# Optimization experiments

Hardware: AMD Instinct MI355X
Metric: run time of the kernel (lower is better)

Reference implementation:

```python
import jax, jax.numpy as jnp
import numpy as np

BETA = 6.0
LOG_2PI = float(np.log(2.0 * np.pi))


def setup_inputs() -> dict:
    key = jax.random.key(0)
    k1, k2, k3, k4 = jax.random.split(key, 4)
    B, L = 2048, 64
    kl = jax.random.uniform(k1, (B, L), dtype=jnp.float32)
    z_mean = jax.random.normal(k2, (B, L), dtype=jnp.float32)
    z_logvar = jax.random.normal(k3, (B, L), dtype=jnp.float32)
    z_sampled = jax.random.normal(k4, (B, L), dtype=jnp.float32)
    return {"kl": kl, "z_mean": z_mean, "z_logvar": z_logvar, "z_sampled": z_sampled}


def gaussian_log_density(samples, mean, log_var):
    # samples: [B,1,L], mean/log_var: [1,B,L] -> [B,B,L]
    tmp = samples - mean
    return -0.5 * (tmp * tmp * jnp.exp(-log_var) + log_var + LOG_2PI)


def total_correlation(z, z_mean, z_logvar):
    # [B, B, L]: log q(z_i_l | x_j)
    log_qz_prob = gaussian_log_density(z[:, None, :], z_mean[None, :, :], z_logvar[None, :, :])
    # sum_l logsumexp_j -> [B]
    log_qz_product = jnp.sum(jax.scipy.special.logsumexp(log_qz_prob, axis=1), axis=1)
    # logsumexp_j sum_l -> [B]
    log_qz = jax.scipy.special.logsumexp(jnp.sum(log_qz_prob, axis=2), axis=1)
    return jnp.mean(log_qz - log_qz_product)


def reference(kl, z_mean, z_logvar, z_sampled):
    kl_loss = jnp.sum(kl)
    tc = (BETA - 1.0) * total_correlation(z_sampled, z_mean, z_logvar)
    return tc + kl_loss
```

## Files before the change

### kernel.cpp

```cpp
#include <hip/hip_runtime.h>
#include <math.h>


#define NB 2048
#define NL 64
#define NE (NB * NL)
#define BVAL 12.0f

__device__ __forceinline__ float wredsum(float v) {
#pragma unroll
  for (int o = 32; o; o >>= 1) v += __shfl_xor(v, o, 64);
  return v;
}
__device__ __forceinline__ float wredmax(float v) {
#pragma unroll
  for (int o = 32; o; o >>= 1) v = fmaxf(v, __shfl_xor(v, o, 64));
  return v;
}

__global__ __launch_bounds__(256) void k1_pre(const float* __restrict__ kl,
                                              const float* __restrict__ zm,
                                              const float* __restrict__ zlv,
                                              float4* __restrict__ PK2,
                                              float* __restrict__ A2T,
                                              float* __restrict__ MA2T,
                                              float* __restrict__ QC2,
                                              float* __restrict__ KLP) {
  const float INVLN2 = 1.4426950408889634f;
  const float LOG2PI = 1.8378770664093453f;
  int tid = threadIdx.x;
  int e = blockIdx.x * 256 + tid;
  int j = e >> 6, l = e & 63;
  float lv = zlv[e], m = zm[e];
  float a2 = -0.5f * INVLN2 * __expf(-lv);
  float b2 = -0.5f * INVLN2 * (lv + LOG2PI);
  float c1 = -2.0f * a2 * m;
  float c0 = fmaf(a2 * m, m, b2);
  PK2[e] = make_float4(a2, c1, c0 - BVAL, 0.0f);
  A2T[l * NB + j] = a2;
  MA2T[l * NB + j] = c1;
  float q = wredsum(c0);
  if (l == 0) QC2[j] = q;
  float ks = wredsum(kl[e]);
  __shared__ float sk[4];
  if (l == 0) sk[tid >> 6] = ks;
  __syncthreads();
  if (tid == 0) KLP[blockIdx.x] = sk[0] + sk[1] + sk[2] + sk[3];
}

__global__ __launch_bounds__(256) void k2_t(const float* __restrict__ zs,
                                            const float* __restrict__ A2T,
                                            const float* __restrict__ MA2T,
                                            const float* __restrict__ QC2,
                                            float* __restrict__ TPM,
                                            float* __restrict__ TPS) {
  int jc = blockIdx.x;
  int i0 = blockIdx.y * 8;
  int tid = threadIdx.x;
  int w = tid >> 6;
  int j = jc * 256 + tid;
  __shared__ float zsh[64][8];
  if (tid < 128) {
    int k = tid >> 1, r0 = (tid & 1) * 4;
#pragma unroll
    for (int r = 0; r < 4; ++r) zsh[k][r0 + r] = zs[(i0 + r0 + r) * NL + k];
  }
  __syncthreads();
  float accv[8];
  float q = QC2[j];
#pragma unroll
  for (int r = 0; r < 8; ++r) accv[r] = q;
  for (int k = 0; k < 64; ++k) {
    float av = A2T[k * NB + j];
    float mv = MA2T[k * NB + j];
    const float4* z4 = (const float4*)&zsh[k][0];
    float4 za = z4[0], zb = z4[1];
    float zk[8] = {za.x, za.y, za.z, za.w, zb.x, zb.y, zb.z, zb.w};
#pragma unroll
    for (int r = 0; r < 8; ++r) {
      accv[r] = fmaf(zk[r] * zk[r], av, accv[r]);
      accv[r] = fmaf(zk[r], mv, accv[r]);
    }
  }
  __shared__ float lm[4][8], ls[4][8];
#pragma unroll
  for (int r = 0; r < 8; ++r) {
    float mx = wredmax(accv[r]);
    if ((tid & 63) == 0) lm[w][r] = mx;
  }
  __syncthreads();
  float Mt[8];
#pragma unroll
  for (int r = 0; r < 8; ++r)
    Mt[r] = fmaxf(fmaxf(lm[0][r], lm[1][r]), fmaxf(lm[2][r], lm[3][r]));
#pragma unroll
  for (int r = 0; r < 8; ++r) {
    float ss = wredsum(__builtin_amdgcn_exp2f(accv[r] - Mt[r]));
    if ((tid & 63) == 0) ls[w][r] = ss;
  }
  __syncthreads();
  if (tid == 0) {
#pragma unroll
    for (int r = 0; r < 8; ++r) {
      TPM[(i0 + r) * 8 + jc] = Mt[r];
      TPS[(i0 + r) * 8 + jc] = ls[0][r] + ls[1][r] + ls[2][r] + ls[3][r];
    }
  }
}

__global__ __launch_bounds__(256) void k3_lse(const float* __restrict__ zs,
                                              const float4* __restrict__ PK2,
                                              float* __restrict__ SP) {
  int jc = blockIdx.x;
  int i0 = blockIdx.y * 8;
  int tid = threadIdx.x;
  int w = tid >> 6, l = tid & 63;
  const float4* p = PK2 + (size_t)(jc * 256 + w * 64) * NL + l;
  float zr[8];
#pragma unroll
  for (int r = 0; r < 8; ++r) zr[r] = zs[(i0 + r) * NL + l];
  float S[8];
#pragma unroll
  for (int r = 0; r < 8; ++r) S[r] = 0.0f;
#pragma unroll 4
  for (int jj = 0; jj < 64; ++jj) {
    float4 c = p[(size_t)jj * NL];
#pragma unroll
    for (int r = 0; r < 8; ++r) {
      float lp2 = fmaf(fmaf(zr[r], c.x, c.y), zr[r], c.z);
      S[r] += __builtin_amdgcn_exp2f(lp2);
    }
  }
  __shared__ float lss[4][8][64];
#pragma unroll
  for (int r = 0; r < 8; ++r) lss[w][r][l] = S[r];
  __syncthreads();
  for (int pp = tid; pp < 512; pp += 256) {
    int r = pp >> 6, ll = pp & 63;
    float Sc = lss[0][r][ll] + lss[1][r][ll] + lss[2][r][ll] + lss[3][r][ll];
    SP[((size_t)jc * NB + (i0 + r)) * NL + ll] = Sc;
  }
}

__global__ __launch_bounds__(256) void k4_fin(const float* __restrict__ SP,
                                              const float* __restrict__ TPM,
                                              const float* __restrict__ TPS,
                                              float* __restrict__ PERI) {
  int tid = threadIdx.x;
  int w = tid >> 6, l = tid & 63;
  int i = blockIdx.x * 4 + w;
  float S = 0.0f;
#pragma unroll
  for (int s = 0; s < 8; ++s) S += SP[((size_t)s * NB + i) * NL + l];
  float val = __builtin_amdgcn_logf(S);
  float lqp2 = wredsum(val) + 64.0f * BVAL;
  float tm = (l < 8) ? TPM[i * 8 + l] : -1e30f;
  float ts = (l < 8) ? TPS[i * 8 + l] : 0.0f;
  float Mt = wredmax(tm);
  float St = wredsum(ts * __builtin_amdgcn_exp2f(tm - Mt));
  float lqz2 = Mt + __builtin_amdgcn_logf(St);
  if (l == 0) PERI[i] = lqz2 - lqp2;
}

__global__ __launch_bounds__(256) void k5_out(const float* __restrict__ KLP,
                                              const float* __restrict__ PERI,
                                              float* __restrict__ out) {
  int tid = threadIdx.x;
  float a = 0.0f, b = 0.0f;
  for (int x = tid; x < 512; x += 256) a += KLP[x];
  for (int x = tid; x < 2048; x += 256) b += PERI[x];
  float ra = wredsum(a), rb = wredsum(b);
  __shared__ float sa[4], sb[4];
  if ((tid & 63) == 0) {
    sa[tid >> 6] = ra;
    sb[tid >> 6] = rb;
  }
  __syncthreads();
  if (tid == 0) {
    const float LN2 = 0.6931471805599453f;
    float ka = sa[0] + sa[1] + sa[2] + sa[3];
    float kb = sb[0] + sb[1] + sb[2] + sb[3];
    out[0] = ka + 5.0f * LN2 * kb * (1.0f / (float)NB);
  }
}

extern "C" void kernel_launch(void* const* d_in, const int* in_sizes, int n_in,
                              void* d_out, int out_size, void* d_ws, size_t ws_size,
                              hipStream_t stream) {
  const float* kl = (const float*)d_in[0];
  const float* zm = (const float*)d_in[1];
  const float* zlv = (const float*)d_in[2];
  const float* zs = (const float*)d_in[3];
  float* ws = (float*)d_ws;

  float* PK2 = ws;
  float* A2T = PK2 + 4 * NE;
  float* MA2T = A2T + NE;
  float* QC2 = MA2T + NE;
  float* SP = QC2 + NB;
  float* TPM = SP + 8 * NE;
  float* TPS = TPM + NB * 8;
  float* KLP = TPS + NB * 8;
  float* PERI = KLP + 512;

  k1_pre<<<NE / 256, 256, 0, stream>>>(kl, zm, zlv, (float4*)PK2, A2T, MA2T, QC2, KLP);
  k2_t<<<dim3(8, NB / 8), 256, 0, stream>>>(zs, A2T, MA2T, QC2, TPM, TPS);
  k3_lse<<<dim3(8, NB / 8), 256, 0, stream>>>(zs, (const float4*)PK2, SP);
  k4_fin<<<NB / 4, 256, 0, stream>>>(SP, TPM, TPS, PERI);
  k5_out<<<1, 256, 0, stream>>>(KLP, PERI, (float*)d_out);
}
```

Baseline: 135.0 us.

## Fuse TC, LSE, finalize and output kernels with atomic last-block reductions

Merges the four post-processing kernels into one launch. The joint-density pass and the per-dimension logsumexp pass now share a block over a larger tile of 16 sample rows, where each block previously handled 8. The per-row finalization and the global output reduction run in whichever block arrives last, detected with atomic counters and threadfences. This removes three kernel launches and their gaps and doubles reuse of the loaded coefficients per block. In exchange it raises register pressure, since 16 accumulators are held per thread, and halves the grid size, which may reduce occupancy and parallelism.

```diff
diff --git a/kernel.cpp b/kernel.cpp
--- a/kernel.cpp
+++ b/kernel.cpp
@@ -6,6 +6,8 @@
 #define NL 64
 #define NE (NB * NL)
 #define BVAL 12.0f
+#define ITILE 16
+#define NTILE (NB / ITILE)
 
 __device__ __forceinline__ float wredsum(float v) {
 #pragma unroll
@@ -25,12 +27,14 @@
                                               float* __restrict__ A2T,
                                               float* __restrict__ MA2T,
                                               float* __restrict__ QC2,
-                                              float* __restrict__ KLP) {
+                                              float* __restrict__ KLP,
+                                              int* __restrict__ CNT) {
   const float INVLN2 = 1.4426950408889634f;
   const float LOG2PI = 1.8378770664093453f;
   int tid = threadIdx.x;
   int e = blockIdx.x * 256 + tid;
   int j = e >> 6, l = e & 63;
+  if (e < NTILE + 1) CNT[e] = 0;
   float lv = zlv[e], m = zm[e];
   float a2 = -0.5f * INVLN2 * __expf(-lv);
   float b2 = -0.5f * INVLN2 * (lv + LOG2PI);
@@ -48,133 +52,143 @@
   if (tid == 0) KLP[blockIdx.x] = sk[0] + sk[1] + sk[2] + sk[3];
 }
 
-__global__ __launch_bounds__(256) void k2_t(const float* __restrict__ zs,
-                                            const float* __restrict__ A2T,
-                                            const float* __restrict__ MA2T,
-                                            const float* __restrict__ QC2,
-                                            float* __restrict__ TPM,
-                                            float* __restrict__ TPS) {
+__global__ __launch_bounds__(256) void k23(const float* __restrict__ zs,
+                                           const float* __restrict__ A2T,
+                                           const float* __restrict__ MA2T,
+                                           const float* __restrict__ QC2,
+                                           const float4* __restrict__ PK2,
+                                           float* __restrict__ TPM,
+                                           float* __restrict__ TPS,
+                                           float* __restrict__ SP,
+                                           const float* __restrict__ KLP,
+                                           float* __restrict__ PERI,
+                                           int* __restrict__ CNT,
+                                           float* __restrict__ out) {
   int jc = blockIdx.x;
-  int i0 = blockIdx.y * 8;
+  int it = blockIdx.y;
+  int i0 = it * ITILE;
   int tid = threadIdx.x;
-  int w = tid >> 6;
+  int w = tid >> 6, l = tid & 63;
   int j = jc * 256 + tid;
-  __shared__ float zsh[64][8];
-  if (tid < 128) {
-    int k = tid >> 1, r0 = (tid & 1) * 4;
-#pragma unroll
-    for (int r = 0; r < 4; ++r) zsh[k][r0 + r] = zs[(i0 + r0 + r) * NL + k];
-  }
-  __syncthreads();
-  float accv[8];
+
+  __shared__ float zsh[64][ITILE];
+  __shared__ float lm[4][ITILE], ls[4][ITILE];
+  __shared__ float lss[4][ITILE][64];
+  __shared__ float sa[4], sb[4];
+  __shared__ int bcast;
+
+  for (int idx = tid; idx < 64 * ITILE; idx += 256) {
+    int r = idx >> 6, k = idx & 63;
+    zsh[k][r] = zs[(i0 + r) * NL + k];
+  }
+  __syncthreads();
+
   float q = QC2[j];
-#pragma unroll
-  for (int r = 0; r < 8; ++r) accv[r] = q;
+  float accv[ITILE];
+#pragma unroll
+  for (int r = 0; r < ITILE; ++r) accv[r] = q;
   for (int k = 0; k < 64; ++k) {
     float av = A2T[k * NB + j];
     float mv = MA2T[k * NB + j];
     const float4* z4 = (const float4*)&zsh[k][0];
-    float4 za = z4[0], zb = z4[1];
-    float zk[8] = {za.x, za.y, za.z, za.w, zb.x, zb.y, zb.z, zb.w};
-#pragma unroll
-    for (int r = 0; r < 8; ++r) {
-      accv[r] = fmaf(zk[r] * zk[r], av, accv[r]);
-      accv[r] = fmaf(zk[r], mv, accv[r]);
-    }
-  }
-  __shared__ float lm[4][8], ls[4][8];
-#pragma unroll
-  for (int r = 0; r < 8; ++r) {
-    float mx = wredmax(accv[r]);
-    if ((tid & 63) == 0) lm[w][r] = mx;
-  }
-  __syncthreads();
-  float Mt[8];
-#pragma unroll
-  for (int r = 0; r < 8; ++r)
-    Mt[r] = fmaxf(fmaxf(lm[0][r], lm[1][r]), fmaxf(lm[2][r], lm[3][r]));
-#pragma unroll
-  for (int r = 0; r < 8; ++r) {
-    float ss = wredsum(__builtin_amdgcn_exp2f(accv[r] - Mt[r]));
-    if ((tid & 63) == 0) ls[w][r] = ss;
-  }
-  __syncthreads();
-  if (tid == 0) {
-#pragma unroll
-    for (int r = 0; r < 8; ++r) {
-      TPM[(i0 + r) * 8 + jc] = Mt[r];
-      TPS[(i0 + r) * 8 + jc] = ls[0][r] + ls[1][r] + ls[2][r] + ls[3][r];
-    }
-  }
-}
-
-__global__ __launch_bounds__(256) void k3_lse(const float* __restrict__ zs,
-                                              const float4* __restrict__ PK2,
-                                              float* __restrict__ SP) {
-  int jc = blockIdx.x;
-  int i0 = blockIdx.y * 8;
-  int tid = threadIdx.x;
-  int w = tid >> 6, l = tid & 63;
+#pragma unroll
+    for (int r4 = 0; r4 < ITILE / 4; ++r4) {
+      float4 zq = z4[r4];
+      float zk[4] = {zq.x, zq.y, zq.z, zq.w};
+#pragma unroll
+      for (int rr = 0; rr < 4; ++rr) {
+        int r = r4 * 4 + rr;
+        accv[r] = fmaf(zk[rr] * zk[rr], av, accv[r]);
+        accv[r] = fmaf(zk[rr], mv, accv[r]);
+      }
+    }
+  }
+  {
+    float Mt[ITILE];
+#pragma unroll
+    for (int r = 0; r < ITILE; ++r) {
+      float mx = wredmax(accv[r]);
+      if (l == 0) lm[w][r] = mx;
+    }
+    __syncthreads();
+#pragma unroll
+    for (int r = 0; r < ITILE; ++r)
+      Mt[r] = fmaxf(fmaxf(lm[0][r], lm[1][r]), fmaxf(lm[2][r], lm[3][r]));
+#pragma unroll
+    for (int r = 0; r < ITILE; ++r) {
+      float ss = wredsum(__builtin_amdgcn_exp2f(accv[r] - Mt[r]));
+      if (l == 0) ls[w][r] = ss;
+    }
+    __syncthreads();
+    if (tid == 0) {
+#pragma unroll
+      for (int r = 0; r < ITILE; ++r) {
+        TPM[(i0 + r) * 8 + jc] = Mt[r];
+        TPS[(i0 + r) * 8 + jc] = ls[0][r] + ls[1][r] + ls[2][r] + ls[3][r];
+      }
+    }
+  }
+
+  float zr[ITILE], S[ITILE];
+#pragma unroll
+  for (int r = 0; r < ITILE; ++r) zr[r] = zs[(i0 + r) * NL + l];
+#pragma unroll
+  for (int r = 0; r < ITILE; ++r) S[r] = 0.0f;
   const float4* p = PK2 + (size_t)(jc * 256 + w * 64) * NL + l;
-  float zr[8];
-#pragma unroll
-  for (int r = 0; r < 8; ++r) zr[r] = zs[(i0 + r) * NL + l];
-  float S[8];
-#pragma unroll
-  for (int r = 0; r < 8; ++r) S[r] = 0.0f;
 #pragma unroll 4
   for (int jj = 0; jj < 64; ++jj) {
     float4 c = p[(size_t)jj * NL];
 #pragma unroll
-    for (int r = 0; r < 8; ++r) {
+    for (int r = 0; r < ITILE; ++r) {
       float lp2 = fmaf(fmaf(zr[r], c.x, c.y), zr[r], c.z);
       S[r] += __builtin_amdgcn_exp2f(lp2);
     }
   }
-  __shared__ float lss[4][8][64];
-#pragma unroll
-  for (int r = 0; r < 8; ++r) lss[w][r][l] = S[r];
-  __syncthreads();
-  for (int pp = tid; pp < 512; pp += 256) {
+  __syncthreads();
+#pragma unroll
+  for (int r = 0; r < ITILE; ++r) lss[w][r][l] = S[r];
+  __syncthreads();
+  for (int pp = tid; pp < ITILE * 64; pp += 256) {
     int r = pp >> 6, ll = pp & 63;
     float Sc = lss[0][r][ll] + lss[1][r][ll] + lss[2][r][ll] + lss[3][r][ll];
     SP[((size_t)jc * NB + (i0 + r)) * NL + ll] = Sc;
   }
-}
-
-__global__ __launch_bounds__(256) void k4_fin(const float* __restrict__ SP,
-                                              const float* __restrict__ TPM,
-                                              const float* __restrict__ TPS,
-                                              float* __restrict__ PERI) {
-  int tid = threadIdx.x;
-  int w = tid >> 6, l = tid & 63;
-  int i = blockIdx.x * 4 + w;
-  float S = 0.0f;
-#pragma unroll
-  for (int s = 0; s < 8; ++s) S += SP[((size_t)s * NB + i) * NL + l];
-  float val = __builtin_amdgcn_logf(S);
-  float lqp2 = wredsum(val) + 64.0f * BVAL;
-  float tm = (l < 8) ? TPM[i * 8 + l] : -1e30f;
-  float ts = (l < 8) ? TPS[i * 8 + l] : 0.0f;
-  float Mt = wredmax(tm);
-  float St = wredsum(ts * __builtin_amdgcn_exp2f(tm - Mt));
-  float lqz2 = Mt + __builtin_amdgcn_logf(St);
-  if (l == 0) PERI[i] = lqz2 - lqp2;
-}
-
-__global__ __launch_bounds__(256) void k5_out(const float* __restrict__ KLP,
-                                              const float* __restrict__ PERI,
-                                              float* __restrict__ out) {
-  int tid = threadIdx.x;
+
+  __threadfence();
+  __syncthreads();
+  if (tid == 0) bcast = atomicAdd(&CNT[it], 1);
+  __syncthreads();
+  if (bcast != 7) return;
+  __threadfence();
+
+#pragma unroll
+  for (int rr = 0; rr < 4; ++rr) {
+    int i = i0 + w * 4 + rr;
+    float Sv = 0.0f;
+#pragma unroll
+    for (int s = 0; s < 8; ++s) Sv += SP[((size_t)s * NB + i) * NL + l];
+    float val = __builtin_amdgcn_logf(Sv);
+    float lqp2 = wredsum(val) + 64.0f * BVAL;
+    float tm = (l < 8) ? TPM[i * 8 + l] : -1e30f;
+    float ts = (l < 8) ? TPS[i * 8 + l] : 0.0f;
+    float Mtt = wredmax(tm);
+    float St = wredsum(ts * __builtin_amdgcn_exp2f(tm - Mtt));
+    float lqz2 = Mtt + __builtin_amdgcn_logf(St);
+    if (l == 0) PERI[i] = lqz2 - lqp2;
+  }
+
+  __threadfence();
+  __syncthreads();
+  if (tid == 0) bcast = atomicAdd(&CNT[NTILE], 1);
+  __syncthreads();
+  if (bcast != NTILE - 1) return;
+  __threadfence();
+
   float a = 0.0f, b = 0.0f;
   for (int x = tid; x < 512; x += 256) a += KLP[x];
-  for (int x = tid; x < 2048; x += 256) b += PERI[x];
+  for (int x = tid; x < NB; x += 256) b += PERI[x];
   float ra = wredsum(a), rb = wredsum(b);
-  __shared__ float sa[4], sb[4];
-  if ((tid & 63) == 0) {
-    sa[tid >> 6] = ra;
-    sb[tid >> 6] = rb;
-  }
+  if (l == 0) { sa[w] = ra; sb[w] = rb; }
   __syncthreads();
   if (tid == 0) {
     const float LN2 = 0.6931471805599453f;
@@ -202,10 +216,11 @@
   float* TPS = TPM + NB * 8;
   float* KLP = TPS + NB * 8;
   float* PERI = KLP + 512;
-
-  k1_pre<<<NE / 256, 256, 0, stream>>>(kl, zm, zlv, (float4*)PK2, A2T, MA2T, QC2, KLP);
-  k2_t<<<dim3(8, NB / 8), 256, 0, stream>>>(zs, A2T, MA2T, QC2, TPM, TPS);
-  k3_lse<<<dim3(8, NB / 8), 256, 0, stream>>>(zs, (const float4*)PK2, SP);
-  k4_fin<<<NB / 4, 256, 0, stream>>>(SP, TPM, TPS, PERI);
-  k5_out<<<1, 256, 0, stream>>>(KLP, PERI, (float*)d_out);
-}
+  int* CNT = (int*)(PERI + NB);
+
+  k1_pre<<<NE / 256, 256, 0, stream>>>(kl, zm, zlv, (float4*)PK2, A2T, MA2T,
+                                       QC2, KLP, CNT);
+  k23<<<dim3(8, NTILE), 256, 0, stream>>>(zs, A2T, MA2T, QC2, (const float4*)PK2,
+                                          TPM, TPS, SP, KLP, PERI, CNT,
+                                          (float*)d_out);
+}
```

Result: slower. 286.8 us (+112.5%).
